# Kernel tuning notes

Hardware: AMD Instinct MI355X
Metric: run time of the kernel (lower is better)

## Reference

```python
import jax, jax.numpy as jnp
import numpy as np

NUM_EXPERTS = 12
TOP_K = 2
FFN_DIM = 1280
HIDDEN = 2048


def setup_inputs() -> dict:
    key = jax.random.key(0)
    k0, k1, k2, k3, k4 = jax.random.split(key, 5)
    B, S, H, F, E = 4, 1024, HIDDEN, FFN_DIM, NUM_EXPERTS
    hidden_states = jax.random.normal(k0, (B, S, H), dtype=jnp.float32)
    # single gate actually used (cluster_index_count=0 -> cluster_index_list[-1])
    gate_w = jax.random.normal(k1, (E, H), dtype=jnp.float32) * 0.02
    w1 = jax.random.normal(k2, (E, F, H), dtype=jnp.float32) * 0.02  # f1: H->F
    w2 = jax.random.normal(k3, (E, H, F), dtype=jnp.float32) * 0.02  # f2: F->H
    w3 = jax.random.normal(k4, (E, F, H), dtype=jnp.float32) * 0.02  # f3: H->F
    return {"hidden_states": hidden_states, "gate_w": gate_w, "w1": w1, "w2": w2, "w3": w3}


def reference(hidden_states, gate_w, w1, w2, w3):
    B, S, H = hidden_states.shape
    x = hidden_states.reshape(-1, H)                       # [T, H]
    T = x.shape[0]
    logits = x @ gate_w.T                                  # [T, E]
    probs = jax.nn.softmax(logits, axis=-1)
    top_w, top_i = jax.lax.top_k(probs, TOP_K)             # [T, 2]
    top_w = top_w / jnp.sum(top_w, axis=-1, keepdims=True)
    # dense combine weights [T, E]: routing weight if expert selected else 0
    cw = jnp.zeros((T, NUM_EXPERTS), dtype=x.dtype)
    cw = cw.at[jnp.arange(T)[:, None], top_i].add(top_w)
    out = jnp.zeros_like(x)
    for e in range(NUM_EXPERTS):  # fixed small expert loop
        h = jax.nn.silu(x @ w1[e].T) * (x @ w3[e].T)       # SwiGLU [T, F]
        out = out + (h @ w2[e].T) * cw[:, e:e + 1]
    return out.reshape(B, S, H)
```

## Files before the change

### kernel.cpp

```cpp
#include <hip/hip_runtime.h>

#define T_TOK 4096
#define H_DIM 2048
#define F_DIM 1280
#define NE 12
#define TOTAL_ROWS (2 * T_TOK)

typedef float f32x4 __attribute__((ext_vector_type(4)));
typedef short bf16x8 __attribute__((ext_vector_type(8)));

__device__ __forceinline__ unsigned short f2bf(float f) {
    unsigned int u = __float_as_uint(f);
    u += 0x7FFFu + ((u >> 16) & 1u);
    return (unsigned short)(u >> 16);
}

__device__ __forceinline__ void gl2lds16(const void* g, void* l) {
    __builtin_amdgcn_global_load_lds(
        (const __attribute__((address_space(1))) unsigned int*)g,
        (__attribute__((address_space(3))) unsigned int*)l,
        16, 0, 0);
}

__global__ __launch_bounds__(256) void convert_kernel(
    const float* __restrict__ src, unsigned short* __restrict__ dst)
{
    size_t i = ((size_t)blockIdx.x * 256 + threadIdx.x) * 8;
    float4 a = *(const float4*)(src + i);
    float4 b = *(const float4*)(src + i + 4);
    unsigned short o[8];
    o[0] = f2bf(a.x); o[1] = f2bf(a.y); o[2] = f2bf(a.z); o[3] = f2bf(a.w);
    o[4] = f2bf(b.x); o[5] = f2bf(b.y); o[6] = f2bf(b.z); o[7] = f2bf(b.w);
    *(uint4*)(dst + i) = *(const uint4*)o;
}

__global__ __launch_bounds__(256) void gate_kernel(
    const float* __restrict__ x, const float* __restrict__ gw,
    int* __restrict__ counts, int* __restrict__ top_e, float* __restrict__ top_w)
{
    int gid = blockIdx.x * blockDim.x + threadIdx.x;
    int tok = gid >> 6;
    int lane = threadIdx.x & 63;
    if (tok >= T_TOK) return;
    const float* xr = x + (size_t)tok * H_DIM;
    float4 xs[8];
#pragma unroll
    for (int c = 0; c < 8; ++c) xs[c] = *(const float4*)(xr + c * 256 + lane * 4);
    float acc[NE];
#pragma unroll
    for (int e = 0; e < NE; ++e) {
        const float* gr = gw + (size_t)e * H_DIM;
        float s = 0.f;
#pragma unroll
        for (int c = 0; c < 8; ++c) {
            float4 g = *(const float4*)(gr + c * 256 + lane * 4);
            s += xs[c].x * g.x + xs[c].y * g.y + xs[c].z * g.z + xs[c].w * g.w;
        }
        acc[e] = s;
    }
#pragma unroll
    for (int e = 0; e < NE; ++e) {
#pragma unroll
        for (int off = 32; off > 0; off >>= 1)
            acc[e] += __shfl_xor(acc[e], off, 64);
    }
    if (lane == 0) {
        int b0 = 0;
#pragma unroll
        for (int e = 1; e < NE; ++e) if (acc[e] > acc[b0]) b0 = e;
        int b1 = (b0 == 0) ? 1 : 0;
#pragma unroll
        for (int e = 0; e < NE; ++e) if (e != b0 && acc[e] > acc[b1]) b1 = e;
        float t = __expf(acc[b1] - acc[b0]);
        float w0 = 1.f / (1.f + t);
        top_e[tok * 2] = b0; top_e[tok * 2 + 1] = b1;
        top_w[tok * 2] = w0; top_w[tok * 2 + 1] = 1.f - w0;
        atomicAdd(&counts[b0], 1);
        atomicAdd(&counts[b1], 1);
    }
}

__global__ void scan_kernel(const int* __restrict__ counts, int* __restrict__ offsets,
                            int* __restrict__ cursors)
{
    if (threadIdx.x == 0 && blockIdx.x == 0) {
        int s = 0;
        for (int e = 0; e < NE; ++e) { offsets[e] = s; s += counts[e]; cursors[e] = 0; }
        offsets[NE] = s;
    }
}

__global__ __launch_bounds__(256) void scatter_kernel(
    const int* __restrict__ top_e, const float* __restrict__ top_w,
    const int* __restrict__ offsets, int* __restrict__ cursors,
    int* __restrict__ row_token, float* __restrict__ row_weight,
    int* __restrict__ inv_pos)
{
    int t = blockIdx.x * blockDim.x + threadIdx.x;
    if (t >= T_TOK) return;
#pragma unroll
    for (int s = 0; s < 2; ++s) {
        int e = top_e[t * 2 + s];
        int pos = atomicAdd(&cursors[e], 1);
        int r = offsets[e] + pos;
        row_token[r] = t;
        row_weight[r] = top_w[t * 2 + s];
        inv_pos[t * 2 + s] = r;
    }
}

__global__ __launch_bounds__(256) void ffn1_kernel(
    const unsigned short* __restrict__ xb, const unsigned short* __restrict__ w1b,
    const unsigned short* __restrict__ w3b,
    const int* __restrict__ counts, const int* __restrict__ offsets,
    const int* __restrict__ row_token, unsigned short* __restrict__ hbuf)
{
    int e = blockIdx.z;
    int cnt = counts[e];
    int m0 = blockIdx.y * 128;
    if (m0 >= cnt) return;
    int base = offsets[e];
    int n0 = blockIdx.x * 128;

    __shared__ unsigned short As[128 * 32];
    __shared__ unsigned short B1s[128 * 32];
    __shared__ unsigned short B3s[128 * 32];

    int t = threadIdx.x;
    int lane = t & 63;
    int wid = t >> 6;
    int wm = wid >> 1, wn = wid & 1;
    int lr = lane & 15, lq = lane >> 4;

    int srow = t >> 2;
    int chunk = t & 3;
    int tok0 = row_token[base + min(m0 + srow, cnt - 1)];
    int tok1 = row_token[base + min(m0 + 64 + srow, cnt - 1)];
    const unsigned short* gA0 = xb + (size_t)tok0 * H_DIM + chunk * 8;
    const unsigned short* gA1 = xb + (size_t)tok1 * H_DIM + chunk * 8;
    const unsigned short* gB1 = w1b + ((size_t)e * F_DIM + n0 + srow) * H_DIM + chunk * 8;
    const unsigned short* gB3 = w3b + ((size_t)e * F_DIM + n0 + srow) * H_DIM + chunk * 8;
    const size_t rowskip = (size_t)64 * H_DIM;

    unsigned short* lA0 = As + wid * 512;
    unsigned short* lA1 = As + 2048 + wid * 512;
    unsigned short* lB10 = B1s + wid * 512;
    unsigned short* lB11 = B1s + 2048 + wid * 512;
    unsigned short* lB30 = B3s + wid * 512;
    unsigned short* lB31 = B3s + 2048 + wid * 512;

    f32x4 acc1[4][4] = {};
    f32x4 acc3[4][4] = {};

    for (int k0 = 0; k0 < H_DIM; k0 += 32) {
        gl2lds16(gA0 + k0, lA0);
        gl2lds16(gA1 + k0, lA1);
        gl2lds16(gB1 + k0, lB10);
        gl2lds16(gB1 + rowskip + k0, lB11);
        gl2lds16(gB3 + k0, lB30);
        gl2lds16(gB3 + rowskip + k0, lB31);
        __syncthreads();

        bf16x8 af[4];
#pragma unroll
        for (int ms = 0; ms < 4; ++ms)
            af[ms] = *(const bf16x8*)(As + (wm * 64 + ms * 16 + lr) * 32 + lq * 8);
#pragma unroll
        for (int ns = 0; ns < 4; ++ns) {
            bf16x8 b1 = *(const bf16x8*)(B1s + (wn * 64 + ns * 16 + lr) * 32 + lq * 8);
            bf16x8 b3 = *(const bf16x8*)(B3s + (wn * 64 + ns * 16 + lr) * 32 + lq * 8);
#pragma unroll
            for (int ms = 0; ms < 4; ++ms) {
                acc1[ms][ns] = __builtin_amdgcn_mfma_f32_16x16x32_bf16(af[ms], b1, acc1[ms][ns], 0, 0, 0);
                acc3[ms][ns] = __builtin_amdgcn_mfma_f32_16x16x32_bf16(af[ms], b3, acc3[ms][ns], 0, 0, 0);
            }
        }
        __syncthreads();
    }

#pragma unroll
    for (int ms = 0; ms < 4; ++ms) {
#pragma unroll
        for (int i = 0; i < 4; ++i) {
            int r = wm * 64 + ms * 16 + lq * 4 + i;
            if (m0 + r < cnt) {
                size_t rowoff = (size_t)(base + m0 + r) * F_DIM;
#pragma unroll
                for (int ns = 0; ns < 4; ++ns) {
                    int c = n0 + wn * 64 + ns * 16 + lr;
                    float a = acc1[ms][ns][i];
                    float hv = (a / (1.f + __expf(-a))) * acc3[ms][ns][i];
                    hbuf[rowoff + c] = f2bf(hv);
                }
            }
        }
    }
}

__global__ __launch_bounds__(256) void ffn2_kernel(
    const unsigned short* __restrict__ hbuf, const unsigned short* __restrict__ w2b,
    const int* __restrict__ counts, const int* __restrict__ offsets,
    const float* __restrict__ row_weight, float* __restrict__ ybuf)
{
    int e = blockIdx.z;
    int cnt = counts[e];
    int m0 = blockIdx.y * 128;
    if (m0 >= cnt) return;
    int base = offsets[e];
    int n0 = blockIdx.x * 128;

    __shared__ unsigned short As[128 * 32];
    __shared__ unsigned short Bs[128 * 32];

    int t = threadIdx.x;
    int lane = t & 63;
    int wid = t >> 6;
    int wm = wid >> 1, wn = wid & 1;
    int lr = lane & 15, lq = lane >> 4;

    int srow = t >> 2;
    int chunk = t & 3;
    const unsigned short* gA0 = hbuf + (size_t)(base + min(m0 + srow, cnt - 1)) * F_DIM + chunk * 8;
    const unsigned short* gA1 = hbuf + (size_t)(base + min(m0 + 64 + srow, cnt - 1)) * F_DIM + chunk * 8;
    const unsigned short* gB = w2b + ((size_t)e * H_DIM + n0 + srow) * F_DIM + chunk * 8;
    const size_t rowskip = (size_t)64 * F_DIM;

    unsigned short* lA0 = As + wid * 512;
    unsigned short* lA1 = As + 2048 + wid * 512;
    unsigned short* lB0 = Bs + wid * 512;
    unsigned short* lB1 = Bs + 2048 + wid * 512;

    f32x4 acc[4][4] = {};

    for (int k0 = 0; k0 < F_DIM; k0 += 32) {
        gl2lds16(gA0 + k0, lA0);
        gl2lds16(gA1 + k0, lA1);
        gl2lds16(gB + k0, lB0);
        gl2lds16(gB + rowskip + k0, lB1);
        __syncthreads();

        bf16x8 af[4];
#pragma unroll
        for (int ms = 0; ms < 4; ++ms)
            af[ms] = *(const bf16x8*)(As + (wm * 64 + ms * 16 + lr) * 32 + lq * 8);
#pragma unroll
        for (int ns = 0; ns < 4; ++ns) {
            bf16x8 b = *(const bf16x8*)(Bs + (wn * 64 + ns * 16 + lr) * 32 + lq * 8);
#pragma unroll
            for (int ms = 0; ms < 4; ++ms)
                acc[ms][ns] = __builtin_amdgcn_mfma_f32_16x16x32_bf16(af[ms], b, acc[ms][ns], 0, 0, 0);
        }
        __syncthreads();
    }

#pragma unroll
    for (int ms = 0; ms < 4; ++ms) {
#pragma unroll
        for (int i = 0; i < 4; ++i) {
            int r = wm * 64 + ms * 16 + lq * 4 + i;
            if (m0 + r < cnt) {
                float wgt = row_weight[base + m0 + r];
                size_t rowoff = (size_t)(base + m0 + r) * H_DIM;
#pragma unroll
                for (int ns = 0; ns < 4; ++ns) {
                    int c = n0 + wn * 64 + ns * 16 + lr;
                    ybuf[rowoff + c] = acc[ms][ns][i] * wgt;
                }
            }
        }
    }
}

__global__ __launch_bounds__(256) void combine_kernel(
    const float* __restrict__ ybuf, const int* __restrict__ inv_pos,
    float* __restrict__ out)
{
    int tk = blockIdx.x;
    int p0 = inv_pos[2 * tk];
    int p1 = inv_pos[2 * tk + 1];
    const float4* y0 = (const float4*)(ybuf + (size_t)p0 * H_DIM);
    const float4* y1 = (const float4*)(ybuf + (size_t)p1 * H_DIM);
    float4* o = (float4*)(out + (size_t)tk * H_DIM);
#pragma unroll
    for (int i = threadIdx.x; i < H_DIM / 4; i += 256) {
        float4 a = y0[i], b = y1[i];
        float4 r;
        r.x = a.x + b.x; r.y = a.y + b.y; r.z = a.z + b.z; r.w = a.w + b.w;
        o[i] = r;
    }
}

extern "C" void kernel_launch(void* const* d_in, const int* in_sizes, int n_in,
                              void* d_out, int out_size, void* d_ws, size_t ws_size,
                              hipStream_t stream)
{
    const float* x  = (const float*)d_in[0];
    const float* gw = (const float*)d_in[1];
    const float* w1 = (const float*)d_in[2];
    const float* w2 = (const float*)d_in[3];
    const float* w3 = (const float*)d_in[4];
    float* out = (float*)d_out;

    unsigned char* p = (unsigned char*)d_ws;
    int* counts     = (int*)p;  p += 256;
    int* cursors    = (int*)p;  p += 256;
    int* offsets    = (int*)p;  p += 256;
    int* top_e      = (int*)p;  p += 2 * T_TOK * 4;
    float* top_w    = (float*)p; p += 2 * T_TOK * 4;
    int* row_token  = (int*)p;  p += 2 * T_TOK * 4;
    float* row_weight = (float*)p; p += 2 * T_TOK * 4;
    int* inv_pos    = (int*)p;  p += 2 * T_TOK * 4;
    unsigned short* xb  = (unsigned short*)p; p += (size_t)T_TOK * H_DIM * 2;
    unsigned short* w2b = (unsigned short*)p; p += (size_t)NE * H_DIM * F_DIM * 2;
    unsigned short* hb  = (unsigned short*)p; p += (size_t)TOTAL_ROWS * F_DIM * 2;
    unsigned short* w1b = (unsigned short*)p;
    unsigned short* w3b = (unsigned short*)(p + (size_t)NE * F_DIM * H_DIM * 2);
    float* ybuf = (float*)p;

    const int WELEM = NE * F_DIM * H_DIM;
    convert_kernel<<<T_TOK * H_DIM / 2048, 256, 0, stream>>>(x, xb);
    convert_kernel<<<WELEM / 2048, 256, 0, stream>>>(w1, w1b);
    convert_kernel<<<WELEM / 2048, 256, 0, stream>>>(w2, w2b);
    convert_kernel<<<WELEM / 2048, 256, 0, stream>>>(w3, w3b);

    hipMemsetAsync(counts, 0, 64 * sizeof(int), stream);
    gate_kernel<<<T_TOK / 4, 256, 0, stream>>>(x, gw, counts, top_e, top_w);
    scan_kernel<<<1, 64, 0, stream>>>(counts, offsets, cursors);
    scatter_kernel<<<T_TOK / 256, 256, 0, stream>>>(top_e, top_w, offsets, cursors,
                                                    row_token, row_weight, inv_pos);

    dim3 g1(F_DIM / 128, 32, NE);
    ffn1_kernel<<<g1, 256, 0, stream>>>(xb, w1b, w3b, counts, offsets, row_token, hb);

    dim3 g2(H_DIM / 128, 32, NE);
    ffn2_kernel<<<g2, 256, 0, stream>>>(hb, w2b, counts, offsets, row_weight, ybuf);

    combine_kernel<<<T_TOK, 256, 0, stream>>>(ybuf, inv_pos, out);
}
```

Before: 833.0 us.

## Double-buffer LDS tiles in both FFN GEMM kernels to overlap loads with MFMA

Both expert GEMM kernels now keep two LDS buffers per operand. The global-to-LDS load for the next K step is issued before the MFMAs on the current buffer, which removes one barrier per iteration and hides load latency behind compute. Launch bounds now request 3 blocks per CU, which limits registers per thread. The doubled LDS footprint and the register cap risk lower occupancy or spills. There is also a correctness concern: the prefetch writes the other buffer before the barrier, and the loop relies on the end-of-iteration barrier for safety. No vmcnt wait precedes that barrier, so the async LDS writes may not be complete when the next iteration reads them.

Result: faster. 785.9 us (-5.7%).

```diff
diff --git a/kernel.cpp b/kernel.cpp
--- a/kernel.cpp
+++ b/kernel.cpp
@@ -109,7 +109,7 @@
     }
 }
 
-__global__ __launch_bounds__(256) void ffn1_kernel(
+__global__ __launch_bounds__(256, 3) void ffn1_kernel(
     const unsigned short* __restrict__ xb, const unsigned short* __restrict__ w1b,
     const unsigned short* __restrict__ w3b,
     const int* __restrict__ counts, const int* __restrict__ offsets,
@@ -122,9 +122,9 @@
     int base = offsets[e];
     int n0 = blockIdx.x * 128;
 
-    __shared__ unsigned short As[128 * 32];
-    __shared__ unsigned short B1s[128 * 32];
-    __shared__ unsigned short B3s[128 * 32];
+    __shared__ unsigned short As[2][128 * 32];
+    __shared__ unsigned short B1s[2][128 * 32];
+    __shared__ unsigned short B3s[2][128 * 32];
 
     int t = threadIdx.x;
     int lane = t & 63;
@@ -142,33 +142,43 @@
     const unsigned short* gB3 = w3b + ((size_t)e * F_DIM + n0 + srow) * H_DIM + chunk * 8;
     const size_t rowskip = (size_t)64 * H_DIM;
 
-    unsigned short* lA0 = As + wid * 512;
-    unsigned short* lA1 = As + 2048 + wid * 512;
-    unsigned short* lB10 = B1s + wid * 512;
-    unsigned short* lB11 = B1s + 2048 + wid * 512;
-    unsigned short* lB30 = B3s + wid * 512;
-    unsigned short* lB31 = B3s + 2048 + wid * 512;
+    int sbase = wid * 512;
 
     f32x4 acc1[4][4] = {};
     f32x4 acc3[4][4] = {};
 
+#define FFN1_STAGE(buf, kk)                                        \
+    do {                                                           \
+        gl2lds16(gA0 + (kk), &As[buf][sbase]);                     \
+        gl2lds16(gA1 + (kk), &As[buf][2048 + sbase]);              \
+        gl2lds16(gB1 + (kk), &B1s[buf][sbase]);                    \
+        gl2lds16(gB1 + rowskip + (kk), &B1s[buf][2048 + sbase]);   \
+        gl2lds16(gB3 + (kk), &B3s[buf][sbase]);                    \
+        gl2lds16(gB3 + rowskip + (kk), &B3s[buf][2048 + sbase]);   \
+    } while (0)
+
+    FFN1_STAGE(0, 0);
+    __syncthreads();
+
+    int cur = 0;
+    int aoff = (wm * 64 + lr) * 32 + lq * 8;
+    int boff = (wn * 64 + lr) * 32 + lq * 8;
+
     for (int k0 = 0; k0 < H_DIM; k0 += 32) {
-        gl2lds16(gA0 + k0, lA0);
-        gl2lds16(gA1 + k0, lA1);
-        gl2lds16(gB1 + k0, lB10);
-        gl2lds16(gB1 + rowskip + k0, lB11);
-        gl2lds16(gB3 + k0, lB30);
-        gl2lds16(gB3 + rowskip + k0, lB31);
-        __syncthreads();
+        if (k0 + 32 < H_DIM) FFN1_STAGE(cur ^ 1, k0 + 32);
+
+        const unsigned short* Ac  = As[cur];
+        const unsigned short* B1c = B1s[cur];
+        const unsigned short* B3c = B3s[cur];
 
         bf16x8 af[4];
 #pragma unroll
         for (int ms = 0; ms < 4; ++ms)
-            af[ms] = *(const bf16x8*)(As + (wm * 64 + ms * 16 + lr) * 32 + lq * 8);
+            af[ms] = *(const bf16x8*)(Ac + aoff + ms * 16 * 32);
 #pragma unroll
         for (int ns = 0; ns < 4; ++ns) {
-            bf16x8 b1 = *(const bf16x8*)(B1s + (wn * 64 + ns * 16 + lr) * 32 + lq * 8);
-            bf16x8 b3 = *(const bf16x8*)(B3s + (wn * 64 + ns * 16 + lr) * 32 + lq * 8);
+            bf16x8 b1 = *(const bf16x8*)(B1c + boff + ns * 16 * 32);
+            bf16x8 b3 = *(const bf16x8*)(B3c + boff + ns * 16 * 32);
 #pragma unroll
             for (int ms = 0; ms < 4; ++ms) {
                 acc1[ms][ns] = __builtin_amdgcn_mfma_f32_16x16x32_bf16(af[ms], b1, acc1[ms][ns], 0, 0, 0);
@@ -176,7 +186,9 @@
             }
         }
         __syncthreads();
-    }
+        cur ^= 1;
+    }
+#undef FFN1_STAGE
 
 #pragma unroll
     for (int ms = 0; ms < 4; ++ms) {
@@ -197,7 +209,7 @@
     }
 }
 
-__global__ __launch_bounds__(256) void ffn2_kernel(
+__global__ __launch_bounds__(256, 3) void ffn2_kernel(
     const unsigned short* __restrict__ hbuf, const unsigned short* __restrict__ w2b,
     const int* __restrict__ counts, const int* __restrict__ offsets,
     const float* __restrict__ row_weight, float* __restrict__ ybuf)
@@ -209,8 +221,8 @@
     int base = offsets[e];
     int n0 = blockIdx.x * 128;
 
-    __shared__ unsigned short As[128 * 32];
-    __shared__ unsigned short Bs[128 * 32];
+    __shared__ unsigned short As[2][128 * 32];
+    __shared__ unsigned short Bs[2][128 * 32];
 
     int t = threadIdx.x;
     int lane = t & 63;
@@ -225,33 +237,46 @@
     const unsigned short* gB = w2b + ((size_t)e * H_DIM + n0 + srow) * F_DIM + chunk * 8;
     const size_t rowskip = (size_t)64 * F_DIM;
 
-    unsigned short* lA0 = As + wid * 512;
-    unsigned short* lA1 = As + 2048 + wid * 512;
-    unsigned short* lB0 = Bs + wid * 512;
-    unsigned short* lB1 = Bs + 2048 + wid * 512;
+    int sbase = wid * 512;
 
     f32x4 acc[4][4] = {};
 
+#define FFN2_STAGE(buf, kk)                                      \
+    do {                                                         \
+        gl2lds16(gA0 + (kk), &As[buf][sbase]);                   \
+        gl2lds16(gA1 + (kk), &As[buf][2048 + sbase]);            \
+        gl2lds16(gB + (kk), &Bs[buf][sbase]);                    \
+        gl2lds16(gB + rowskip + (kk), &Bs[buf][2048 + sbase]);   \
+    } while (0)
+
+    FFN2_STAGE(0, 0);
+    __syncthreads();
+
+    int cur = 0;
+    int aoff = (wm * 64 + lr) * 32 + lq * 8;
+    int boff = (wn * 64 + lr) * 32 + lq * 8;
+
     for (int k0 = 0; k0 < F_DIM; k0 += 32) {
-        gl2lds16(gA0 + k0, lA0);
-        gl2lds16(gA1 + k0, lA1);
-        gl2lds16(gB + k0, lB0);
-        gl2lds16(gB + rowskip + k0, lB1);
-        __syncthreads();
+        if (k0 + 32 < F_DIM) FFN2_STAGE(cur ^ 1, k0 + 32);
+
+        const unsigned short* Ac = As[cur];
+        const unsigned short* Bc = Bs[cur];
 
         bf16x8 af[4];
 #pragma unroll
         for (int ms = 0; ms < 4; ++ms)
-            af[ms] = *(const bf16x8*)(As + (wm * 64 + ms * 16 + lr) * 32 + lq * 8);
+            af[ms] = *(const bf16x8*)(Ac + aoff + ms * 16 * 32);
 #pragma unroll
         for (int ns = 0; ns < 4; ++ns) {
-            bf16x8 b = *(const bf16x8*)(Bs + (wn * 64 + ns * 16 + lr) * 32 + lq * 8);
+            bf16x8 b = *(const bf16x8*)(Bc + boff + ns * 16 * 32);
 #pragma unroll
             for (int ms = 0; ms < 4; ++ms)
                 acc[ms][ns] = __builtin_amdgcn_mfma_f32_16x16x32_bf16(af[ms], b, acc[ms][ns], 0, 0, 0);
         }
         __syncthreads();
-    }
+        cur ^= 1;
+    }
+#undef FFN2_STAGE
 
 #pragma unroll
     for (int ms = 0; ms < 4; ++ms) {
```

## Double-buffer expert GEMMs with swizzled LDS and interleaved w1/w3 weights

Applied to the files above, without the earlier changes.

Both expert GEMM kernels become 512-thread blocks with 128x256 tiles, a K step of 64 and double-buffered LDS filled by async global-to-LDS loads, waited on with explicit vmcnt counts. LDS reads are XOR-swizzled to avoid bank conflicts, and MFMA sections run at raised wave priority. The w1 and w3 weights are converted into one interleaved matrix in 16-row groups, so ffn1 runs as a single GEMM and pairs adjacent accumulator tiles for SwiGLU. The larger LDS footprint may reduce occupancy, and the hand-set waitcnt depends on the exact load count per stage.

New measurement: 809.0 us. 2.9% less time.

```diff
diff --git a/kernel.cpp b/kernel.cpp
--- a/kernel.cpp
+++ b/kernel.cpp
@@ -5,6 +5,7 @@
 #define F_DIM 1280
 #define NE 12
 #define TOTAL_ROWS (2 * T_TOK)
+#define NCAT (2 * F_DIM)
 
 typedef float f32x4 __attribute__((ext_vector_type(4)));
 typedef short bf16x8 __attribute__((ext_vector_type(8)));
@@ -34,6 +35,22 @@
     *(uint4*)(dst + i) = *(const uint4*)o;
 }
 
+__global__ __launch_bounds__(256) void convert_w13_kernel(
+    const float* __restrict__ src, unsigned short* __restrict__ wcat, int which)
+{
+    int f = blockIdx.y;
+    int e = blockIdx.z;
+    int dstrow = ((f >> 4) << 5) + which * 16 + (f & 15);
+    size_t si = ((size_t)e * F_DIM + f) * H_DIM + threadIdx.x * 8;
+    size_t di = ((size_t)e * NCAT + dstrow) * H_DIM + threadIdx.x * 8;
+    float4 a = *(const float4*)(src + si);
+    float4 b = *(const float4*)(src + si + 4);
+    unsigned short o[8];
+    o[0] = f2bf(a.x); o[1] = f2bf(a.y); o[2] = f2bf(a.z); o[3] = f2bf(a.w);
+    o[4] = f2bf(b.x); o[5] = f2bf(b.y); o[6] = f2bf(b.z); o[7] = f2bf(b.w);
+    *(uint4*)(wcat + di) = *(const uint4*)o;
+}
+
 __global__ __launch_bounds__(256) void gate_kernel(
     const float* __restrict__ x, const float* __restrict__ gw,
     int* __restrict__ counts, int* __restrict__ top_e, float* __restrict__ top_w)
@@ -109,9 +126,10 @@
     }
 }
 
-__global__ __launch_bounds__(256) void ffn1_kernel(
-    const unsigned short* __restrict__ xb, const unsigned short* __restrict__ w1b,
-    const unsigned short* __restrict__ w3b,
+#define NT1 (H_DIM / 64)
+
+__global__ __launch_bounds__(512, 2) void ffn1_kernel(
+    const unsigned short* __restrict__ xb, const unsigned short* __restrict__ wcat,
     const int* __restrict__ counts, const int* __restrict__ offsets,
     const int* __restrict__ row_token, unsigned short* __restrict__ hbuf)
 {
@@ -120,64 +138,90 @@
     int m0 = blockIdx.y * 128;
     if (m0 >= cnt) return;
     int base = offsets[e];
-    int n0 = blockIdx.x * 128;
-
-    __shared__ unsigned short As[128 * 32];
-    __shared__ unsigned short B1s[128 * 32];
-    __shared__ unsigned short B3s[128 * 32];
+    int n0 = blockIdx.x * 256;
+
+    __shared__ unsigned short As[2][128 * 64];
+    __shared__ unsigned short Bs[2][256 * 64];
 
     int t = threadIdx.x;
     int lane = t & 63;
-    int wid = t >> 6;
-    int wm = wid >> 1, wn = wid & 1;
+    int w = t >> 6;
+    int wm = w >> 2, wn = w & 3;
     int lr = lane & 15, lq = lane >> 4;
-
-    int srow = t >> 2;
-    int chunk = t & 3;
-    int tok0 = row_token[base + min(m0 + srow, cnt - 1)];
-    int tok1 = row_token[base + min(m0 + 64 + srow, cnt - 1)];
-    const unsigned short* gA0 = xb + (size_t)tok0 * H_DIM + chunk * 8;
-    const unsigned short* gA1 = xb + (size_t)tok1 * H_DIM + chunk * 8;
-    const unsigned short* gB1 = w1b + ((size_t)e * F_DIM + n0 + srow) * H_DIM + chunk * 8;
-    const unsigned short* gB3 = w3b + ((size_t)e * F_DIM + n0 + srow) * H_DIM + chunk * 8;
-    const size_t rowskip = (size_t)64 * H_DIM;
-
-    unsigned short* lA0 = As + wid * 512;
-    unsigned short* lA1 = As + 2048 + wid * 512;
-    unsigned short* lB10 = B1s + wid * 512;
-    unsigned short* lB11 = B1s + 2048 + wid * 512;
-    unsigned short* lB30 = B3s + wid * 512;
-    unsigned short* lB31 = B3s + 2048 + wid * 512;
-
-    f32x4 acc1[4][4] = {};
-    f32x4 acc3[4][4] = {};
-
-    for (int k0 = 0; k0 < H_DIM; k0 += 32) {
-        gl2lds16(gA0 + k0, lA0);
-        gl2lds16(gA1 + k0, lA1);
-        gl2lds16(gB1 + k0, lB10);
-        gl2lds16(gB1 + rowskip + k0, lB11);
-        gl2lds16(gB3 + k0, lB30);
-        gl2lds16(gB3 + rowskip + k0, lB31);
-        __syncthreads();
-
-        bf16x8 af[4];
-#pragma unroll
-        for (int ms = 0; ms < 4; ++ms)
-            af[ms] = *(const bf16x8*)(As + (wm * 64 + ms * 16 + lr) * 32 + lq * 8);
-#pragma unroll
-        for (int ns = 0; ns < 4; ++ns) {
-            bf16x8 b1 = *(const bf16x8*)(B1s + (wn * 64 + ns * 16 + lr) * 32 + lq * 8);
-            bf16x8 b3 = *(const bf16x8*)(B3s + (wn * 64 + ns * 16 + lr) * 32 + lq * 8);
-#pragma unroll
-            for (int ms = 0; ms < 4; ++ms) {
-                acc1[ms][ns] = __builtin_amdgcn_mfma_f32_16x16x32_bf16(af[ms], b1, acc1[ms][ns], 0, 0, 0);
-                acc3[ms][ns] = __builtin_amdgcn_mfma_f32_16x16x32_bf16(af[ms], b3, acc3[ms][ns], 0, 0, 0);
-            }
+    int x7 = lr & 7;
+
+    int r8 = lane >> 3;
+    int schunk = (lane & 7) ^ r8;
+
+    const unsigned short* gA[2];
+#pragma unroll
+    for (int j = 0; j < 2; ++j) {
+        int rl = w * 16 + j * 8 + r8;
+        int tok = row_token[base + min(m0 + rl, cnt - 1)];
+        gA[j] = xb + (size_t)tok * H_DIM + schunk * 8;
+    }
+    const unsigned short* gB[4];
+#pragma unroll
+    for (int j = 0; j < 4; ++j) {
+        int rl = w * 32 + j * 8 + r8;
+        gB[j] = wcat + ((size_t)e * NCAT + n0 + rl) * H_DIM + schunk * 8;
+    }
+
+    int arow[4], brow[4], sl[2];
+#pragma unroll
+    for (int ms = 0; ms < 4; ++ms) arow[ms] = (wm * 64 + ms * 16 + lr) * 64;
+#pragma unroll
+    for (int ns = 0; ns < 4; ++ns) brow[ns] = (wn * 64 + ns * 16 + lr) * 64;
+    sl[0] = (lq ^ x7) * 8;
+    sl[1] = ((4 + lq) ^ x7) * 8;
+
+    f32x4 acc[4][4] = {};
+
+#define STAGE1(buf, kt)                                            \
+    do {                                                           \
+        int koff = (kt) * 64;                                      \
+        gl2lds16(gA[0] + koff, &As[buf][w * 1024]);                \
+        gl2lds16(gA[1] + koff, &As[buf][w * 1024 + 512]);          \
+        gl2lds16(gB[0] + koff, &Bs[buf][w * 2048]);                \
+        gl2lds16(gB[1] + koff, &Bs[buf][w * 2048 + 512]);          \
+        gl2lds16(gB[2] + koff, &Bs[buf][w * 2048 + 1024]);         \
+        gl2lds16(gB[3] + koff, &Bs[buf][w * 2048 + 1536]);         \
+    } while (0)
+
+    STAGE1(0, 0);
+    STAGE1(1, 1);
+
+    for (int kt = 0; kt < NT1; ++kt) {
+        int cur = kt & 1;
+        if (kt < NT1 - 1) asm volatile("s_waitcnt vmcnt(6)" ::: "memory");
+        else              asm volatile("s_waitcnt vmcnt(0)" ::: "memory");
+        __builtin_amdgcn_s_barrier();
+        __builtin_amdgcn_sched_barrier(0);
+
+        const unsigned short* Ac = As[cur];
+        const unsigned short* Bc = Bs[cur];
+        __builtin_amdgcn_s_setprio(1);
+#pragma unroll
+        for (int ks = 0; ks < 2; ++ks) {
+            bf16x8 af[4], bf[4];
+#pragma unroll
+            for (int ms = 0; ms < 4; ++ms) af[ms] = *(const bf16x8*)(Ac + arow[ms] + sl[ks]);
+#pragma unroll
+            for (int ns = 0; ns < 4; ++ns) bf[ns] = *(const bf16x8*)(Bc + brow[ns] + sl[ks]);
+#pragma unroll
+            for (int ns = 0; ns < 4; ++ns)
+#pragma unroll
+                for (int ms = 0; ms < 4; ++ms)
+                    acc[ms][ns] = __builtin_amdgcn_mfma_f32_16x16x32_bf16(af[ms], bf[ns], acc[ms][ns], 0, 0, 0);
         }
-        __syncthreads();
-    }
-
+        __builtin_amdgcn_s_setprio(0);
+        __builtin_amdgcn_sched_barrier(0);
+        __builtin_amdgcn_s_barrier();
+        if (kt + 2 < NT1) STAGE1(cur, kt + 2);
+    }
+#undef STAGE1
+
+    int hbase = blockIdx.x * 128 + wn * 32;
 #pragma unroll
     for (int ms = 0; ms < 4; ++ms) {
 #pragma unroll
@@ -186,18 +230,20 @@
             if (m0 + r < cnt) {
                 size_t rowoff = (size_t)(base + m0 + r) * F_DIM;
 #pragma unroll
-                for (int ns = 0; ns < 4; ++ns) {
-                    int c = n0 + wn * 64 + ns * 16 + lr;
-                    float a = acc1[ms][ns][i];
-                    float hv = (a / (1.f + __expf(-a))) * acc3[ms][ns][i];
-                    hbuf[rowoff + c] = f2bf(hv);
+                for (int p = 0; p < 2; ++p) {
+                    float a = acc[ms][2 * p][i];
+                    float b = acc[ms][2 * p + 1][i];
+                    float hv = (a / (1.f + __expf(-a))) * b;
+                    hbuf[rowoff + hbase + p * 16 + lr] = f2bf(hv);
                 }
             }
         }
     }
 }
 
-__global__ __launch_bounds__(256) void ffn2_kernel(
+#define NT2 (F_DIM / 64)
+
+__global__ __launch_bounds__(512, 2) void ffn2_kernel(
     const unsigned short* __restrict__ hbuf, const unsigned short* __restrict__ w2b,
     const int* __restrict__ counts, const int* __restrict__ offsets,
     const float* __restrict__ row_weight, float* __restrict__ ybuf)
@@ -207,51 +253,87 @@
     int m0 = blockIdx.y * 128;
     if (m0 >= cnt) return;
     int base = offsets[e];
-    int n0 = blockIdx.x * 128;
-
-    __shared__ unsigned short As[128 * 32];
-    __shared__ unsigned short Bs[128 * 32];
+    int n0 = blockIdx.x * 256;
+
+    __shared__ unsigned short As[2][128 * 64];
+    __shared__ unsigned short Bs[2][256 * 64];
 
     int t = threadIdx.x;
     int lane = t & 63;
-    int wid = t >> 6;
-    int wm = wid >> 1, wn = wid & 1;
+    int w = t >> 6;
+    int wm = w >> 2, wn = w & 3;
     int lr = lane & 15, lq = lane >> 4;
-
-    int srow = t >> 2;
-    int chunk = t & 3;
-    const unsigned short* gA0 = hbuf + (size_t)(base + min(m0 + srow, cnt - 1)) * F_DIM + chunk * 8;
-    const unsigned short* gA1 = hbuf + (size_t)(base + min(m0 + 64 + srow, cnt - 1)) * F_DIM + chunk * 8;
-    const unsigned short* gB = w2b + ((size_t)e * H_DIM + n0 + srow) * F_DIM + chunk * 8;
-    const size_t rowskip = (size_t)64 * F_DIM;
-
-    unsigned short* lA0 = As + wid * 512;
-    unsigned short* lA1 = As + 2048 + wid * 512;
-    unsigned short* lB0 = Bs + wid * 512;
-    unsigned short* lB1 = Bs + 2048 + wid * 512;
+    int x7 = lr & 7;
+
+    int r8 = lane >> 3;
+    int schunk = (lane & 7) ^ r8;
+
+    const unsigned short* gA[2];
+#pragma unroll
+    for (int j = 0; j < 2; ++j) {
+        int rl = w * 16 + j * 8 + r8;
+        gA[j] = hbuf + (size_t)(base + min(m0 + rl, cnt - 1)) * F_DIM + schunk * 8;
+    }
+    const unsigned short* gB[4];
+#pragma unroll
+    for (int j = 0; j < 4; ++j) {
+        int rl = w * 32 + j * 8 + r8;
+        gB[j] = w2b + ((size_t)e * H_DIM + n0 + rl) * F_DIM + schunk * 8;
+    }
+
+    int arow[4], brow[4], sl[2];
+#pragma unroll
+    for (int ms = 0; ms < 4; ++ms) arow[ms] = (wm * 64 + ms * 16 + lr) * 64;
+#pragma unroll
+    for (int ns = 0; ns < 4; ++ns) brow[ns] = (wn * 64 + ns * 16 + lr) * 64;
+    sl[0] = (lq ^ x7) * 8;
+    sl[1] = ((4 + lq) ^ x7) * 8;
 
     f32x4 acc[4][4] = {};
 
-    for (int k0 = 0; k0 < F_DIM; k0 += 32) {
-        gl2lds16(gA0 + k0, lA0);
-        gl2lds16(gA1 + k0, lA1);
-        gl2lds16(gB + k0, lB0);
-        gl2lds16(gB + rowskip + k0, lB1);
-        __syncthreads();
-
-        bf16x8 af[4];
-#pragma unroll
-        for (int ms = 0; ms < 4; ++ms)
-            af[ms] = *(const bf16x8*)(As + (wm * 64 + ms * 16 + lr) * 32 + lq * 8);
-#pragma unroll
-        for (int ns = 0; ns < 4; ++ns) {
-            bf16x8 b = *(const bf16x8*)(Bs + (wn * 64 + ns * 16 + lr) * 32 + lq * 8);
-#pragma unroll
-            for (int ms = 0; ms < 4; ++ms)
-                acc[ms][ns] = __builtin_amdgcn_mfma_f32_16x16x32_bf16(af[ms], b, acc[ms][ns], 0, 0, 0);
+#define STAGE2(buf, kt)                                            \
+    do {                                                           \
+        int koff = (kt) * 64;                                      \
+        gl2lds16(gA[0] + koff, &As[buf][w * 1024]);                \
+        gl2lds16(gA[1] + koff, &As[buf][w * 1024 + 512]);          \
+        gl2lds16(gB[0] + koff, &Bs[buf][w * 2048]);                \
+        gl2lds16(gB[1] + koff, &Bs[buf][w * 2048 + 512]);          \
+        gl2lds16(gB[2] + koff, &Bs[buf][w * 2048 + 1024]);         \
+        gl2lds16(gB[3] + koff, &Bs[buf][w * 2048 + 1536]);         \
+    } while (0)
+
+    STAGE2(0, 0);
+    STAGE2(1, 1);
+
+    for (int kt = 0; kt < NT2; ++kt) {
+        int cur = kt & 1;
+        if (kt < NT2 - 1) asm volatile("s_waitcnt vmcnt(6)" ::: "memory");
+        else              asm volatile("s_waitcnt vmcnt(0)" ::: "memory");
+        __builtin_amdgcn_s_barrier();
+        __builtin_amdgcn_sched_barrier(0);
+
+        const unsigned short* Ac = As[cur];
+        const unsigned short* Bc = Bs[cur];
+        __builtin_amdgcn_s_setprio(1);
+#pragma unroll
+        for (int ks = 0; ks < 2; ++ks) {
+            bf16x8 af[4], bf[4];
+#pragma unroll
+            for (int ms = 0; ms < 4; ++ms) af[ms] = *(const bf16x8*)(Ac + arow[ms] + sl[ks]);
+#pragma unroll
+            for (int ns = 0; ns < 4; ++ns) bf[ns] = *(const bf16x8*)(Bc + brow[ns] + sl[ks]);
+#pragma unroll
+            for (int ns = 0; ns < 4; ++ns)
+#pragma unroll
+                for (int ms = 0; ms < 4; ++ms)
+                    acc[ms][ns] = __builtin_amdgcn_mfma_f32_16x16x32_bf16(af[ms], bf[ns], acc[ms][ns], 0, 0, 0);
         }
-        __syncthreads();
-    }
+        __builtin_amdgcn_s_setprio(0);
+        __builtin_amdgcn_sched_barrier(0);
+        __builtin_amdgcn_s_barrier();
+        if (kt + 2 < NT2) STAGE2(cur, kt + 2);
+    }
+#undef STAGE2
 
 #pragma unroll
     for (int ms = 0; ms < 4; ++ms) {
@@ -313,15 +395,15 @@
     unsigned short* xb  = (unsigned short*)p; p += (size_t)T_TOK * H_DIM * 2;
     unsigned short* w2b = (unsigned short*)p; p += (size_t)NE * H_DIM * F_DIM * 2;
     unsigned short* hb  = (unsigned short*)p; p += (size_t)TOTAL_ROWS * F_DIM * 2;
-    unsigned short* w1b = (unsigned short*)p;
-    unsigned short* w3b = (unsigned short*)(p + (size_t)NE * F_DIM * H_DIM * 2);
+    unsigned short* wcat = (unsigned short*)p;
     float* ybuf = (float*)p;
 
     const int WELEM = NE * F_DIM * H_DIM;
     convert_kernel<<<T_TOK * H_DIM / 2048, 256, 0, stream>>>(x, xb);
-    convert_kernel<<<WELEM / 2048, 256, 0, stream>>>(w1, w1b);
     convert_kernel<<<WELEM / 2048, 256, 0, stream>>>(w2, w2b);
-    convert_kernel<<<WELEM / 2048, 256, 0, stream>>>(w3, w3b);
+    dim3 gw13(1, F_DIM, NE);
+    convert_w13_kernel<<<gw13, 256, 0, stream>>>(w1, wcat, 0);
+    convert_w13_kernel<<<gw13, 256, 0, stream>>>(w3, wcat, 1);
 
     hipMemsetAsync(counts, 0, 64 * sizeof(int), stream);
     gate_kernel<<<T_TOK / 4, 256, 0, stream>>>(x, gw, counts, top_e, top_w);
@@ -329,11 +411,11 @@
     scatter_kernel<<<T_TOK / 256, 256, 0, stream>>>(top_e, top_w, offsets, cursors,
                                                     row_token, row_weight, inv_pos);
 
-    dim3 g1(F_DIM / 128, 32, NE);
-    ffn1_kernel<<<g1, 256, 0, stream>>>(xb, w1b, w3b, counts, offsets, row_token, hb);
-
-    dim3 g2(H_DIM / 128, 32, NE);
-    ffn2_kernel<<<g2, 256, 0, stream>>>(hb, w2b, counts, offsets, row_weight, ybuf);
+    dim3 g1(NCAT / 256, 32, NE);
+    ffn1_kernel<<<g1, 512, 0, stream>>>(xb, wcat, counts, offsets, row_token, hb);
+
+    dim3 g2(H_DIM / 256, 32, NE);
+    ffn2_kernel<<<g2, 512, 0, stream>>>(hb, w2b, counts, offsets, row_weight, ybuf);
 
     combine_kernel<<<T_TOK, 256, 0, stream>>>(ybuf, inv_pos, out);
 }
```
